# Optimization experiments

Measured on AMD Instinct MI355X. Metric: run time of the kernel, lower is better.

## Reference

```python
import jax, jax.numpy as jnp
import numpy as np

N_STARS = 2048   # n_stars
BATCH = 256      # query positions per call
PF = 28          # poly_features = (d_max+1)(d_max+2)/2, d_max=6
NGE = 512        # n_graph_elems
GF = 32          # graph_features
OPD = 256        # opd_dim


def setup_inputs() -> dict:
    key = jax.random.key(0)
    ks = jax.random.split(key, 8)
    # observed star positions in the FoV (x_lims/y_lims = [0,1000])
    obs_pos = jax.random.uniform(ks[0], (N_STARS, 2), jnp.float32, 0.0, 1000.0)
    # query positions are exact rows of obs_pos (required by the exact-match index search)
    idx = jax.random.randint(ks[1], (BATCH,), 0, N_STARS)
    positions = obs_pos[idx]
    poly_dic = jax.random.normal(ks[2], (N_STARS, PF), jnp.float32)
    graph_dic = jax.random.normal(ks[3], (N_STARS, NGE), jnp.float32)
    # alpha matrices: identity(-padded) init as in init_vars, plus small noise
    alpha_poly = jnp.eye(PF, dtype=jnp.float32) + 0.01 * jax.random.normal(ks[4], (PF, PF), jnp.float32)
    alpha_graph = (jnp.eye(NGE, GF, dtype=jnp.float32)
                   + 0.01 * jax.random.normal(ks[5], (NGE, GF), jnp.float32))
    # S features: random uniform in [-1e-3, 1e-3] as in init_vars
    S_poly = jax.random.uniform(ks[6], (PF, OPD, OPD), jnp.float32, -0.001, 0.001)
    S_graph = jax.random.uniform(ks[7], (GF, OPD, OPD), jnp.float32, -0.001, 0.001)
    return {
        'positions': positions, 'obs_pos': obs_pos,
        'poly_dic': poly_dic, 'graph_dic': graph_dic,
        'alpha_poly': alpha_poly, 'alpha_graph': alpha_graph,
        'S_poly': S_poly, 'S_graph': S_graph,
    }


def _calc_indices(positions, obs_pos):
    # Faithful to tf.where(tf.equal(obs_pos, pos))[0, 0]: first True entry (row-major)
    # of the elementwise equality over (n_stars, 2); its row index is taken.
    eq = positions[:, None, :] == obs_pos[None, :, :]          # (B, N, 2) bool
    flat_first = jnp.argmax(eq.reshape(eq.shape[0], -1), axis=1)  # first True, flat index
    return flat_first // 2                                      # row index in obs_pos


def reference(positions, obs_pos, poly_dic, graph_dic, alpha_poly, alpha_graph, S_poly, S_graph):
    indices = _calc_indices(positions, obs_pos)                 # (B,) int
    # polynomial part: gather -> matmul -> tensordot with OPD modes
    batch_poly = jnp.take(poly_dic, indices, axis=0)            # (B, PF)
    interm_poly = batch_poly @ alpha_poly                       # (B, PF)
    contrib_poly = jnp.einsum('bp,pij->bij', interm_poly, S_poly)  # (B, OPD, OPD)
    # graph part
    batch_graph = jnp.take(graph_dic, indices, axis=0)          # (B, NGE)
    interm_graph = batch_graph @ alpha_graph                    # (B, GF)
    contrib_graph = jnp.einsum('bg,gij->bij', interm_graph, S_graph)
    return contrib_poly + contrib_graph
```

## Files before the change

kernel.cpp:

```cpp
#include <hip/hip_runtime.h>

#define NSTARS 2048
#define BATCH  256
#define PF     28
#define NGE    512
#define GF     32
#define OPD2   65536
#define KTOT   (PF + GF)
#define TM     16
#define KB     4
#define NT     (KTOT / KB)

typedef float f32x4 __attribute__((ext_vector_type(4)));

__global__ __launch_bounds__(256) void prep_kernel(
    const float* __restrict__ positions,  const float* __restrict__ obs_pos,
    const float* __restrict__ poly_dic,   const float* __restrict__ graph_dic,
    const float* __restrict__ alpha_poly, const float* __restrict__ alpha_graph,
    float* __restrict__ Wt)
{
    const int b = blockIdx.x;
    const int t = threadIdx.x;

    const float p0 = positions[2 * b];
    const float p1 = positions[2 * b + 1];

    int cand = 0x7fffffff;
    #pragma unroll
    for (int i = 0; i < NSTARS / 256; ++i) {
        const int n = t + i * 256;
        const float o0 = obs_pos[2 * n];
        const float o1 = obs_pos[2 * n + 1];
        if (o0 == p0 || o1 == p1) cand = min(cand, n);
    }
    __shared__ int smin[256];
    smin[t] = cand;
    __syncthreads();
    for (int s = 128; s > 0; s >>= 1) {
        if (t < s) smin[t] = min(smin[t], smin[t + s]);
        __syncthreads();
    }
    int idx = smin[0];
    if (idx == 0x7fffffff) idx = 0;

    if (t < PF) {
        float acc = 0.f;
        #pragma unroll
        for (int p = 0; p < PF; ++p)
            acc += poly_dic[idx * PF + p] * alpha_poly[p * PF + t];
        Wt[t * BATCH + b] = acc;
    }

    __shared__ float psum[8][GF];
    {
        const int g = t & 31;
        const int r = t >> 5;
        float acc = 0.f;
        const int e0 = r * (NGE / 8);
        for (int e = e0; e < e0 + NGE / 8; ++e)
            acc += graph_dic[idx * NGE + e] * alpha_graph[e * GF + g];
        psum[r][g] = acc;
    }
    __syncthreads();
    if (t < GF) {
        float acc = 0.f;
        #pragma unroll
        for (int r = 0; r < 8; ++r) acc += psum[r][t];
        Wt[(PF + t) * BATCH + b] = acc;
    }
}

__global__ __launch_bounds__(256) void main_kernel(
    const float* __restrict__ S_poly, const float* __restrict__ S_graph,
    const float* __restrict__ Wt, float* __restrict__ out)
{
    __shared__ float sbuf[2][KB][1024];

    const int t    = threadIdx.x;
    const int id   = blockIdx.x;
    const int xcd  = id & 7;
    const int slot = id >> 3;
    const int xb   = xcd * 8 + (slot & 7);
    const int yb   = slot >> 3;

    const int ij = xb * 1024 + t * 4;
    const int b0 = yb * TM;

    const float* __restrict__ wp = Wt + b0;

    f32x4 acc[TM];
    #pragma unroll
    for (int b = 0; b < TM; ++b) acc[b] = (f32x4)(0.f);

    const int wbase = (t >> 6) << 8;

    auto stage = [&](int T, int d) {
        const int kb = T * KB;
        const float* base = (T < PF / KB)
            ? (S_poly  + (size_t)kb * OPD2)
            : (S_graph + (size_t)(kb - PF) * OPD2);
        const float* src = base + xb * 1024 + t * 4;
        #pragma unroll
        for (int kk = 0; kk < KB; ++kk) {
            __builtin_amdgcn_global_load_lds(
                (const __attribute__((address_space(1))) uint32_t*)(src + (size_t)kk * OPD2),
                (__attribute__((address_space(3))) uint32_t*)&sbuf[d][kk][wbase],
                16, 0, 0);
        }
    };

    stage(0, 0);
    asm volatile("s_waitcnt vmcnt(0)" ::: "memory");
    __syncthreads();

    int cur = 0;
    for (int T = 0; T < NT; ++T) {
        if (T + 1 < NT) stage(T + 1, cur ^ 1);

        const int kb = T * KB;
        #pragma unroll
        for (int kk = 0; kk < KB; ++kk) {
            const f32x4 s = *reinterpret_cast<const f32x4*>(&sbuf[cur][kk][t * 4]);
            #pragma unroll
            for (int b = 0; b < TM; ++b) {
                const float w = wp[(kb + kk) * BATCH + b];
                acc[b].x = fmaf(w, s.x, acc[b].x);
                acc[b].y = fmaf(w, s.y, acc[b].y);
                acc[b].z = fmaf(w, s.z, acc[b].z);
                acc[b].w = fmaf(w, s.w, acc[b].w);
            }
        }

        asm volatile("s_waitcnt vmcnt(0)" ::: "memory");
        __syncthreads();
        cur ^= 1;
    }

    #pragma unroll
    for (int b = 0; b < TM; ++b) {
        __builtin_nontemporal_store(
            acc[b],
            reinterpret_cast<f32x4*>(out + (size_t)(b0 + b) * OPD2 + ij));
    }
}

extern "C" void kernel_launch(void* const* d_in, const int* in_sizes, int n_in,
                              void* d_out, int out_size, void* d_ws, size_t ws_size,
                              hipStream_t stream) {
    const float* positions   = (const float*)d_in[0];
    const float* obs_pos     = (const float*)d_in[1];
    const float* poly_dic    = (const float*)d_in[2];
    const float* graph_dic   = (const float*)d_in[3];
    const float* alpha_poly  = (const float*)d_in[4];
    const float* alpha_graph = (const float*)d_in[5];
    const float* S_poly      = (const float*)d_in[6];
    const float* S_graph     = (const float*)d_in[7];
    float* out = (float*)d_out;

    float* Wt = (float*)d_ws;

    prep_kernel<<<BATCH, 256, 0, stream>>>(positions, obs_pos, poly_dic,
                                           graph_dic, alpha_poly, alpha_graph,
                                           Wt);

    main_kernel<<<1024, 256, 0, stream>>>(S_poly, S_graph, Wt, out);
}
```

Before: 126.0 us.

## Stage weights in LDS and deepen S prefetch pipeline without block barriers

Each block now copies its 60x16 slice of the weight matrix into shared memory once, then reads it as vector LDS loads instead of per-element global loads inside the FMA loop. The S-tile pipeline becomes two tiles deep: the next-but-one tile is issued right after the current tile's LDS reads complete. It waits with vmcnt(4) instead of draining all loads. The per-iteration __syncthreads is dropped, which relies on each wave reading only the LDS region its own async loads wrote. This is meant to hide global-load latency and remove barrier stalls, at the cost of slightly more LDS use and tighter reliance on the hardware counter ordering.

```diff
diff --git a/kernel.cpp b/kernel.cpp
--- a/kernel.cpp
+++ b/kernel.cpp
@@ -75,6 +75,7 @@
     const float* __restrict__ Wt, float* __restrict__ out)
 {
     __shared__ float sbuf[2][KB][1024];
+    __shared__ float wlds[KTOT * TM];
 
     const int t    = threadIdx.x;
     const int id   = blockIdx.x;
@@ -86,7 +87,9 @@
     const int ij = xb * 1024 + t * 4;
     const int b0 = yb * TM;
 
-    const float* __restrict__ wp = Wt + b0;
+    for (int i = t; i < KTOT * TM; i += 256)
+        wlds[i] = Wt[(i >> 4) * BATCH + b0 + (i & 15)];
+    __syncthreads();
 
     f32x4 acc[TM];
     #pragma unroll
@@ -99,7 +102,7 @@
         const float* base = (T < PF / KB)
             ? (S_poly  + (size_t)kb * OPD2)
             : (S_graph + (size_t)(kb - PF) * OPD2);
-        const float* src = base + xb * 1024 + t * 4;
+        const float* src = base + ij;
         #pragma unroll
         for (int kk = 0; kk < KB; ++kk) {
             __builtin_amdgcn_global_load_lds(
@@ -109,32 +112,43 @@
         }
     };
 
-    stage(0, 0);
-    asm volatile("s_waitcnt vmcnt(0)" ::: "memory");
-    __syncthreads();
-
-    int cur = 0;
-    for (int T = 0; T < NT; ++T) {
-        if (T + 1 < NT) stage(T + 1, cur ^ 1);
-
-        const int kb = T * KB;
+    auto tile_fma = [&](int T, int buf) {
+        f32x4 sv[KB];
+        #pragma unroll
+        for (int kk = 0; kk < KB; ++kk)
+            sv[kk] = *reinterpret_cast<const f32x4*>(&sbuf[buf][kk][t * 4]);
+        asm volatile("s_waitcnt lgkmcnt(0)" ::: "memory");
+        __builtin_amdgcn_sched_barrier(0);
+        if (T + 2 < NT) stage(T + 2, buf);
         #pragma unroll
         for (int kk = 0; kk < KB; ++kk) {
-            const f32x4 s = *reinterpret_cast<const f32x4*>(&sbuf[cur][kk][t * 4]);
-            #pragma unroll
-            for (int b = 0; b < TM; ++b) {
-                const float w = wp[(kb + kk) * BATCH + b];
-                acc[b].x = fmaf(w, s.x, acc[b].x);
-                acc[b].y = fmaf(w, s.y, acc[b].y);
-                acc[b].z = fmaf(w, s.z, acc[b].z);
-                acc[b].w = fmaf(w, s.w, acc[b].w);
-            }
+            const float* wk = &wlds[(T * KB + kk) * TM];
+            const f32x4 w0 = *reinterpret_cast<const f32x4*>(wk);
+            const f32x4 w1 = *reinterpret_cast<const f32x4*>(wk + 4);
+            const f32x4 w2 = *reinterpret_cast<const f32x4*>(wk + 8);
+            const f32x4 w3 = *reinterpret_cast<const f32x4*>(wk + 12);
+            const f32x4 s  = sv[kk];
+            acc[0]  += w0.x * s;  acc[1]  += w0.y * s;
+            acc[2]  += w0.z * s;  acc[3]  += w0.w * s;
+            acc[4]  += w1.x * s;  acc[5]  += w1.y * s;
+            acc[6]  += w1.z * s;  acc[7]  += w1.w * s;
+            acc[8]  += w2.x * s;  acc[9]  += w2.y * s;
+            acc[10] += w2.z * s;  acc[11] += w2.w * s;
+            acc[12] += w3.x * s;  acc[13] += w3.y * s;
+            acc[14] += w3.z * s;  acc[15] += w3.w * s;
         }
+    };
 
-        asm volatile("s_waitcnt vmcnt(0)" ::: "memory");
-        __syncthreads();
-        cur ^= 1;
+    stage(0, 0);
+    stage(1, 1);
+
+    #pragma unroll 1
+    for (int T = 0; T < NT - 1; ++T) {
+        asm volatile("s_waitcnt vmcnt(4)" ::: "memory");
+        tile_fma(T, T & 1);
     }
+    asm volatile("s_waitcnt vmcnt(0)" ::: "memory");
+    tile_fma(NT - 1, (NT - 1) & 1);
 
     #pragma unroll
     for (int b = 0; b < TM; ++b) {
```

New measurement: 128.3 us. Within noise of the previous version (+1.8%).
